# Kernel tuning notes

Measured on AMD Instinct MI355X. Metric: run time of the kernel, lower is better.

Reference implementation:

```python
import jax, jax.numpy as jnp
import numpy as np

B, L, H = 2, 2048, 2048
DI, N, DTR, K = 4096, 16, 128, 4  # intermediate, state, dt_rank, conv kernel


def setup_inputs() -> dict:
    key = jax.random.key(0)
    ks = jax.random.split(key, 8)
    x = jax.random.normal(ks[0], (B, L, H), jnp.float32)
    in_proj_w = jax.random.normal(ks[1], (2 * DI, H), jnp.float32) * 0.02
    conv1d_w = jax.random.normal(ks[2], (DI, 1, K), jnp.float32) * 0.1
    conv1d_b = jnp.zeros((DI,), jnp.float32)
    x_proj_w = jax.random.normal(ks[3], (DTR + 2 * N, DI), jnp.float32) * 0.02
    bound = DTR ** -0.5
    dt_proj_w = jax.random.uniform(ks[4], (DI, DTR), jnp.float32, -bound, bound)
    # faithful dt bias init: inverse-softplus of dt ~ Uniform-log[0.001, 0.1]
    dt = jnp.exp(jax.random.uniform(ks[5], (DI,), jnp.float32)
                 * (np.log(0.1) - np.log(0.001)) + np.log(0.001))
    dt = jnp.clip(dt, 1e-4)
    dt_proj_b = dt + jnp.log(-jnp.expm1(-dt))
    A_log = jnp.log(jnp.broadcast_to(jnp.arange(1, N + 1, dtype=jnp.float32), (DI, N)))
    D = jnp.ones((DI,), jnp.float32)
    out_proj_w = jax.random.normal(ks[6], (H, DI), jnp.float32) * 0.02
    return dict(x=x, in_proj_w=in_proj_w, conv1d_w=conv1d_w, conv1d_b=conv1d_b,
                x_proj_w=x_proj_w, dt_proj_w=dt_proj_w, dt_proj_b=dt_proj_b,
                A_log=A_log, D=D, out_proj_w=out_proj_w)


def _mamba_forward(x, in_proj_w, conv1d_w, conv1d_b, x_proj_w,
                   dt_proj_w, dt_proj_b, A_log, D, out_proj_w):
    # in_proj -> split into ssm input and gate (res)
    x_and_res = jnp.einsum('blh,eh->ble', x, in_proj_w)          # [B,L,2*DI]
    xi, res = jnp.split(x_and_res, 2, axis=-1)                    # [B,L,DI] each

    # depthwise causal conv1d (kernel K, left-pad K-1, truncated to L)
    xc = jnp.transpose(xi, (0, 2, 1))                             # [B,DI,L]
    xc = jax.lax.conv_general_dilated(
        xc, conv1d_w, window_strides=(1,), padding=((K - 1, 0),),
        dimension_numbers=('NCH', 'OIH', 'NCH'), feature_group_count=DI)
    xc = xc + conv1d_b[None, :, None]
    u = jax.nn.silu(jnp.transpose(xc, (0, 2, 1)))                 # [B,L,DI]

    # selective SSM parameters
    A = -jnp.exp(A_log.astype(jnp.float32))                       # [DI,N]
    x_dbl = jnp.einsum('bld,ed->ble', u, x_proj_w)                # [B,L,DTR+2N]
    dlt, Bm, Cm = jnp.split(x_dbl, [DTR, DTR + N], axis=-1)
    delta = jax.nn.softplus(jnp.einsum('blr,dr->bld', dlt, dt_proj_w) + dt_proj_b)

    # selective scan over time; carry h: [B,DI,N]
    def step(h, inp):
        d_t, B_t, C_t, u_t = inp                                  # [B,DI],[B,N],[B,N],[B,DI]
        dA = jnp.exp(d_t[:, :, None] * A)                         # [B,DI,N]
        h = dA * h + d_t[:, :, None] * B_t[:, None, :] * u_t[:, :, None]
        y_t = jnp.einsum('bdn,bn->bd', h, C_t)
        return h, y_t

    xs = (jnp.transpose(delta, (1, 0, 2)), jnp.transpose(Bm, (1, 0, 2)),
          jnp.transpose(Cm, (1, 0, 2)), jnp.transpose(u, (1, 0, 2)))
    h0 = jnp.zeros((x.shape[0], DI, N), jnp.float32)
    _, ys = jax.lax.scan(step, h0, xs)                            # ys: [L,B,DI]
    y = jnp.transpose(ys, (1, 0, 2)) + u * D.astype(jnp.float32)  # skip via D

    y = y * jax.nn.silu(res)                                      # gate
    return jnp.einsum('bld,hd->blh', y, out_proj_w)               # [B,L,H]


def reference(x, in_proj_w, conv1d_w, conv1d_b, x_proj_w,
              dt_proj_w, dt_proj_b, A_log, D, out_proj_w):
    return _mamba_forward(x, in_proj_w, conv1d_w, conv1d_b, x_proj_w,
                          dt_proj_w, dt_proj_b, A_log, D, out_proj_w)
```

## Files before the change

### kernel.cpp

```cpp
#include <hip/hip_runtime.h>
#include <hip/hip_bf16.h>
#include <stdint.h>

#define DEV static __device__ __forceinline__

typedef __attribute__((ext_vector_type(8))) short short8;
typedef __attribute__((ext_vector_type(4))) float f32x4;
typedef __attribute__((address_space(3))) void lds_void;
typedef __attribute__((address_space(1))) void glb_void;

constexpr int CB = 2, CL = 2048, CH = 2048, CDI = 4096, CN = 16, CDTR = 128;
constexpr int BLR = CB * CL;
constexpr int NC = 32, LC = 64;
constexpr int KSL = 8;

DEV ushort f2b(float f) {
  union { float f; uint32_t u; } v; v.f = f;
  uint32_t u = v.u;
  return (ushort)((u + 0x7fffu + ((u >> 16) & 1u)) >> 16);
}
DEV float b2f(ushort b) {
  union { uint32_t u; float f; } v; v.u = ((uint32_t)b) << 16;
  return v.f;
}
DEV void gload16(const ushort* g, ushort* l) {
  __builtin_amdgcn_global_load_lds((const glb_void*)g, (lds_void*)l, 16, 0, 0);
}

__global__ void cast_kernel(const float* __restrict__ in, ushort* __restrict__ out, int n4) {
  int i = blockIdx.x * blockDim.x + threadIdx.x;
  if (i >= n4) return;
  float4 v = *(const float4*)(in + (size_t)i * 4);
  *(ushort4*)(out + (size_t)i * 4) = make_ushort4(f2b(v.x), f2b(v.y), f2b(v.z), f2b(v.w));
}

__global__ void cast_pad_xproj_kernel(const float* __restrict__ in, ushort* __restrict__ out) {
  int i = blockIdx.x * blockDim.x + threadIdx.x;
  if (i >= (256 * 4096 / 4)) return;
  int idx = i * 4;
  int r = idx >> 12;
  ushort4 o;
  if (r < 160) {
    float4 v = *(const float4*)(in + idx);
    o = make_ushort4(f2b(v.x), f2b(v.y), f2b(v.z), f2b(v.w));
  } else {
    o = make_ushort4(0, 0, 0, 0);
  }
  *(ushort4*)(out + idx) = o;
}

__global__ void conv_silu_kernel(const ushort* __restrict__ xr, const float* __restrict__ w,
                                 const float* __restrict__ bias, ushort* __restrict__ u) {
  int t = blockIdx.x * blockDim.x + threadIdx.x;
  if (t >= BLR * CDI / 2) return;
  int d2 = t & (CDI / 2 - 1);
  int bl = t >> 11;
  int l = bl & (CL - 1);
  int d = d2 << 1;
  float4 w0 = *(const float4*)(w + (size_t)d * 4);
  float4 w1 = *(const float4*)(w + (size_t)d * 4 + 4);
  float wa0[4] = {w0.x, w0.y, w0.z, w0.w};
  float wa1[4] = {w1.x, w1.y, w1.z, w1.w};
  float a0 = bias[d], a1 = bias[d + 1];
#pragma unroll
  for (int k = 0; k < 4; ++k) {
    int ls = l - 3 + k;
    if (ls >= 0) {
      ushort2 xv = *(const ushort2*)(xr + (size_t)(bl - 3 + k) * 8192 + d);
      a0 = fmaf(wa0[k], b2f(xv.x), a0);
      a1 = fmaf(wa1[k], b2f(xv.y), a1);
    }
  }
  float s0 = a0 / (1.f + __expf(-a0));
  float s1 = a1 / (1.f + __expf(-a1));
  *(ushort2*)(u + (size_t)bl * 4096 + d) = make_ushort2(f2b(s0), f2b(s1));
}

template<int EPI>
__global__ __launch_bounds__(256, 4)
void gemm_bt_kernel(const ushort* __restrict__ A, const ushort* __restrict__ Bw,
                    void* __restrict__ Cp, const float* __restrict__ bias,
                    int M, int N, int K) {
  __shared__ ushort sA[128 * 32];
  __shared__ ushort sB[128 * 32];
  const int tid = threadIdx.x;
  const int bm = blockIdx.x, bn = blockIdx.y;
  const int w = tid >> 6, l = tid & 63;
  const int wr = w >> 1, wc = w & 1;
  const int q = l >> 4, r = l & 15;

  f32x4 acc[4][4] = {};

  const ushort* Ab = A + (size_t)bm * 128 * K;
  const ushort* Bb = Bw + (size_t)bn * 128 * K;
  const int nk = K >> 5;
  for (int kt = 0; kt < nk; ++kt) {
    const int k0 = kt << 5;
#pragma unroll
    for (int i = 0; i < 2; ++i) {
      const int chunk = i * 256 + tid;
      const int row = chunk >> 2;
      const int cofs = (chunk & 3) << 3;
      gload16(Ab + (size_t)row * K + k0 + cofs, sA + chunk * 8);
      gload16(Bb + (size_t)row * K + k0 + cofs, sB + chunk * 8);
    }
    __syncthreads();
    short8 af[4], bfg[4];
#pragma unroll
    for (int i = 0; i < 4; ++i) {
      af[i]  = *(const short8*)(sA + (wr * 64 + i * 16 + r) * 32 + q * 8);
      bfg[i] = *(const short8*)(sB + (wc * 64 + i * 16 + r) * 32 + q * 8);
    }
#pragma unroll
    for (int i = 0; i < 4; ++i)
#pragma unroll
      for (int j = 0; j < 4; ++j)
        acc[i][j] = __builtin_amdgcn_mfma_f32_16x16x32_bf16(af[i], bfg[j], acc[i][j], 0, 0, 0);
    __syncthreads();
  }

  const int m0 = bm * 128 + wr * 64;
  const int n0 = bn * 128 + wc * 64;
#pragma unroll
  for (int i = 0; i < 4; ++i) {
#pragma unroll
    for (int j = 0; j < 4; ++j) {
#pragma unroll
      for (int v = 0; v < 4; ++v) {
        const int grow = m0 + i * 16 + q * 4 + v;
        const int gcol = n0 + j * 16 + r;
        const float val = acc[i][j][v];
        if (EPI == 0) {
          ((ushort*)Cp)[(size_t)grow * N + gcol] = f2b(val);
        } else if (EPI == 1) {
          ((float*)Cp)[(size_t)grow * N + gcol] = val;
        } else {
          float xv = val + bias[gcol];
          float sp = xv > 20.f ? xv : log1pf(__expf(xv));
          ((ushort*)Cp)[(size_t)grow * N + gcol] = f2b(sp);
        }
      }
    }
  }
}

__global__ __launch_bounds__(256, 4)
void gemm_btk_kernel(const ushort* __restrict__ A, const ushort* __restrict__ Bw,
                     float* __restrict__ Cpart, int N, int Ktot, int Ksl) {
  __shared__ ushort sA[128 * 32];
  __shared__ ushort sB[128 * 32];
  const int tid = threadIdx.x;
  const int bm = blockIdx.x, bn = blockIdx.y, z = blockIdx.z;
  const int w = tid >> 6, l = tid & 63;
  const int wr = w >> 1, wc = w & 1;
  const int q = l >> 4, r = l & 15;

  f32x4 acc[4][4] = {};

  const ushort* Ab = A + (size_t)bm * 128 * Ktot + z * Ksl;
  const ushort* Bb = Bw + (size_t)bn * 128 * Ktot + z * Ksl;
  const int nk = Ksl >> 5;
  for (int kt = 0; kt < nk; ++kt) {
    const int k0 = kt << 5;
#pragma unroll
    for (int i = 0; i < 2; ++i) {
      const int chunk = i * 256 + tid;
      const int row = chunk >> 2;
      const int cofs = (chunk & 3) << 3;
      gload16(Ab + (size_t)row * Ktot + k0 + cofs, sA + chunk * 8);
      gload16(Bb + (size_t)row * Ktot + k0 + cofs, sB + chunk * 8);
    }
    __syncthreads();
    short8 af[4], bfg[4];
#pragma unroll
    for (int i = 0; i < 4; ++i) {
      af[i]  = *(const short8*)(sA + (wr * 64 + i * 16 + r) * 32 + q * 8);
      bfg[i] = *(const short8*)(sB + (wc * 64 + i * 16 + r) * 32 + q * 8);
    }
#pragma unroll
    for (int i = 0; i < 4; ++i)
#pragma unroll
      for (int j = 0; j < 4; ++j)
        acc[i][j] = __builtin_amdgcn_mfma_f32_16x16x32_bf16(af[i], bfg[j], acc[i][j], 0, 0, 0);
    __syncthreads();
  }

  float* Cz = Cpart + (size_t)z * BLR * N;
  const int m0 = bm * 128 + wr * 64;
  const int n0 = bn * 128 + wc * 64;
#pragma unroll
  for (int i = 0; i < 4; ++i)
#pragma unroll
    for (int j = 0; j < 4; ++j)
#pragma unroll
      for (int v = 0; v < 4; ++v)
        Cz[(size_t)(m0 + i * 16 + q * 4 + v) * N + (n0 + j * 16 + r)] = acc[i][j][v];
}

__global__ __launch_bounds__(256)
void reduce_xdbl_kernel(const float* __restrict__ part, float* __restrict__ xdbl,
                        ushort* __restrict__ dlt) {
  const int i = blockIdx.x * 256 + threadIdx.x;
  const int idx = i * 4;
  const int row = idx >> 8, col = idx & 255;
  float4 s = make_float4(0.f, 0.f, 0.f, 0.f);
#pragma unroll
  for (int z = 0; z < KSL; ++z) {
    float4 v = *(const float4*)(part + (size_t)z * BLR * 256 + idx);
    s.x += v.x; s.y += v.y; s.z += v.z; s.w += v.w;
  }
  *(float4*)(xdbl + idx) = s;
  if (col < 128) {
    *(ushort4*)(dlt + (size_t)row * 128 + col) =
        make_ushort4(f2b(s.x), f2b(s.y), f2b(s.z), f2b(s.w));
  }
}

__global__ __launch_bounds__(256)
void scan_pass1_kernel(const ushort* __restrict__ delta_bf, const ushort* __restrict__ u_bf,
                       const float* __restrict__ xdbl, const float* __restrict__ A_log,
                       float* __restrict__ Hc, float* __restrict__ Ssum) {
  __shared__ float4 sB[LC * 4];
  const int blk = blockIdx.x;
  const int dblk = blk & 15, bc = blk >> 4;
  const int b = bc & (CB - 1), c = bc >> 1;
  const int tid = threadIdx.x;
  const int d = dblk * 256 + tid;
  const size_t rowbase = (size_t)b * CL + c * LC;

  {
    const int rr = tid >> 2, seg = tid & 3;
    sB[tid] = *(const float4*)(xdbl + (rowbase + rr) * 256 + 128 + seg * 4);
  }
  __syncthreads();

  float Ae[16];
#pragma unroll
  for (int n = 0; n < 16; ++n) Ae[n] = -__expf(A_log[(size_t)d * CN + n]);
  float h[16] = {};
  float S = 0.f;
  for (int t = 0; t < LC; ++t) {
    const float dl = b2f(delta_bf[(rowbase + t) * 4096 + d]);
    const float uu = b2f(u_bf[(rowbase + t) * 4096 + d]);
    const float du = dl * uu;
    S += dl;
#pragma unroll
    for (int q = 0; q < 4; ++q) {
      float4 bq = sB[t * 4 + q];
      h[q * 4 + 0] = __expf(Ae[q * 4 + 0] * dl) * h[q * 4 + 0] + du * bq.x;
      h[q * 4 + 1] = __expf(Ae[q * 4 + 1] * dl) * h[q * 4 + 1] + du * bq.y;
      h[q * 4 + 2] = __expf(Ae[q * 4 + 2] * dl) * h[q * 4 + 2] + du * bq.z;
      h[q * 4 + 3] = __expf(Ae[q * 4 + 3] * dl) * h[q * 4 + 3] + du * bq.w;
    }
  }
  float4* Hp = (float4*)(Hc + ((((size_t)c * CB + b) * CDI + d) << 4));
#pragma unroll
  for (int q = 0; q < 4; ++q)
    Hp[q] = make_float4(h[q * 4 + 0], h[q * 4 + 1], h[q * 4 + 2], h[q * 4 + 3]);
  Ssum[((size_t)c * CB + b) * CDI + d] = S;
}

__global__ __launch_bounds__(256)
void scan_pass2_kernel(float* __restrict__ Hc, const float* __restrict__ Ssum,
                       const float* __restrict__ A_log) {
  const int t = blockIdx.x * 256 + threadIdx.x;
  const int n = t & 15, d = (t >> 4) & (CDI - 1), b = t >> 16;
  const float Ae = -__expf(A_log[(size_t)d * CN + n]);
  float h = 0.f;
  for (int c = 1; c < NC; ++c) {
    const size_t idxp = ((size_t)(c - 1) * CB + b) * CDI + d;
    const float P = __expf(Ae * Ssum[idxp]);
    h = P * h + Hc[idxp * 16 + n];
    Hc[idxp * 16 + n] = h;
  }
}

__global__ __launch_bounds__(256)
void scan_pass3_kernel(const ushort* __restrict__ delta_bf, const ushort* __restrict__ u_bf,
                       const float* __restrict__ xdbl, const ushort* __restrict__ xr,
                       const float* __restrict__ A_log, const float* __restrict__ Dvec,
                       const float* __restrict__ Hc, ushort* __restrict__ ybf) {
  __shared__ float4 sB[LC * 4];
  __shared__ float4 sC[LC * 4];
  const int blk = blockIdx.x;
  const int dblk = blk & 15, bc = blk >> 4;
  const int b = bc & (CB - 1), c = bc >> 1;
  const int tid = threadIdx.x;
  const int d = dblk * 256 + tid;
  const size_t rowbase = (size_t)b * CL + c * LC;

  {
    const int rr = tid >> 2, seg = tid & 3;
    sB[tid] = *(const float4*)(xdbl + (rowbase + rr) * 256 + 128 + seg * 4);
    sC[tid] = *(const float4*)(xdbl + (rowbase + rr) * 256 + 144 + seg * 4);
  }
  __syncthreads();

  float Ae[16];
#pragma unroll
  for (int n = 0; n < 16; ++n) Ae[n] = -__expf(A_log[(size_t)d * CN + n]);
  float h[16];
  if (c == 0) {
#pragma unroll
    for (int n = 0; n < 16; ++n) h[n] = 0.f;
  } else {
    const float4* Hp = (const float4*)(Hc + ((((size_t)(c - 1) * CB + b) * CDI + d) << 4));
#pragma unroll
    for (int q = 0; q < 4; ++q) {
      float4 hv = Hp[q];
      h[q * 4 + 0] = hv.x; h[q * 4 + 1] = hv.y; h[q * 4 + 2] = hv.z; h[q * 4 + 3] = hv.w;
    }
  }
  const float Dd = Dvec[d];
  for (int t = 0; t < LC; ++t) {
    const float dl = b2f(delta_bf[(rowbase + t) * 4096 + d]);
    const float uu = b2f(u_bf[(rowbase + t) * 4096 + d]);
    const float du = dl * uu;
    float y = 0.f;
#pragma unroll
    for (int q = 0; q < 4; ++q) {
      float4 bq = sB[t * 4 + q];
      float4 cq = sC[t * 4 + q];
      h[q * 4 + 0] = __expf(Ae[q * 4 + 0] * dl) * h[q * 4 + 0] + du * bq.x;
      h[q * 4 + 1] = __expf(Ae[q * 4 + 1] * dl) * h[q * 4 + 1] + du * bq.y;
      h[q * 4 + 2] = __expf(Ae[q * 4 + 2] * dl) * h[q * 4 + 2] + du * bq.z;
      h[q * 4 + 3] = __expf(Ae[q * 4 + 3] * dl) * h[q * 4 + 3] + du * bq.w;
      y = fmaf(h[q * 4 + 0], cq.x, y);
      y = fmaf(h[q * 4 + 1], cq.y, y);
      y = fmaf(h[q * 4 + 2], cq.z, y);
      y = fmaf(h[q * 4 + 3], cq.w, y);
    }
    const float res = b2f(xr[(rowbase + t) * 8192 + 4096 + d]);
    const float sres = res / (1.f + __expf(-res));
    ybf[(rowbase + t) * 4096 + d] = f2b((y + uu * Dd) * sres);
  }
}

extern "C" void kernel_launch(void* const* d_in, const int* in_sizes, int n_in,
                              void* d_out, int out_size, void* d_ws, size_t ws_size,
                              hipStream_t stream) {
  (void)in_sizes; (void)n_in; (void)out_size; (void)ws_size;
  const float* x       = (const float*)d_in[0];
  const float* in_w    = (const float*)d_in[1];
  const float* conv_w  = (const float*)d_in[2];
  const float* conv_b  = (const float*)d_in[3];
  const float* xproj_w = (const float*)d_in[4];
  const float* dt_w    = (const float*)d_in[5];
  const float* dt_b    = (const float*)d_in[6];
  const float* A_log   = (const float*)d_in[7];
  const float* Dvec    = (const float*)d_in[8];
  const float* out_w   = (const float*)d_in[9];
  float* out = (float*)d_out;
  char* ws = (char*)d_ws;
  const size_t MB = 1u << 20;

  ushort* xb    = (ushort*)(ws);
  float*  Hc    = (float*)(ws);
  ushort* wout  = (ushort*)(ws);
  ushort* wb1   = (ushort*)(ws + 16 * MB);
  ushort* u_bf  = (ushort*)(ws + 16 * MB);
  ushort* xr    = (ushort*)(ws + 48 * MB);
  float*  part  = (float*)(ws + 112 * MB);
  ushort* delta = (ushort*)(ws + 112 * MB);
  ushort* ybf   = (ushort*)(ws + 144 * MB);
  float*  xdbl  = (float*)(ws + 176 * MB);
  ushort* dlt   = (ushort*)(ws + 180 * MB);
  ushort* wxp   = (ushort*)(ws + 181 * MB);
  ushort* wdt   = (ushort*)(ws + 183 * MB);
  float*  Ssum  = (float*)(ws + 184 * MB);

  auto cast = [&](const float* in, ushort* o, int n) {
    cast_kernel<<<(n / 4 + 255) / 256, 256, 0, stream>>>(in, o, n / 4);
  };

  cast(x, xb, BLR * CH);
  cast(in_w, wb1, 2 * CDI * CH);
  gemm_bt_kernel<0><<<dim3(BLR / 128, (2 * CDI) / 128), 256, 0, stream>>>(
      xb, wb1, xr, nullptr, BLR, 2 * CDI, CH);
  conv_silu_kernel<<<(BLR * CDI / 2) / 256, 256, 0, stream>>>(xr, conv_w, conv_b, u_bf);
  cast_pad_xproj_kernel<<<(256 * 4096 / 4) / 256, 256, 0, stream>>>(xproj_w, wxp);
  gemm_btk_kernel<<<dim3(BLR / 128, 2, KSL), 256, 0, stream>>>(
      u_bf, wxp, part, 256, CDI, CDI / KSL);
  reduce_xdbl_kernel<<<(BLR * 256 / 4) / 256, 256, 0, stream>>>(part, xdbl, dlt);
  cast(dt_w, wdt, CDI * CDTR);
  gemm_bt_kernel<2><<<dim3(BLR / 128, CDI / 128), 256, 0, stream>>>(
      dlt, wdt, delta, dt_b, BLR, CDI, CDTR);
  scan_pass1_kernel<<<NC * CB * (CDI / 256), 256, 0, stream>>>(
      delta, u_bf, xdbl, A_log, Hc, Ssum);
  scan_pass2_kernel<<<(CB * CDI * CN) / 256, 256, 0, stream>>>(Hc, Ssum, A_log);
  scan_pass3_kernel<<<NC * CB * (CDI / 256), 256, 0, stream>>>(
      delta, u_bf, xdbl, xr, A_log, Dvec, Hc, ybf);
  cast(out_w, wout, CH * CDI);
  gemm_bt_kernel<1><<<dim3(BLR / 128, CH / 128), 256, 0, stream>>>(
      ybf, wout, out, nullptr, BLR, CH, CDI);
}
```

Before: 583.8 us.

## Use 256x256 double-buffered pipelined GEMM with swizzled LDS for in_proj

Adds a new 512-thread GEMM kernel with 256x256 output tiles, K-step 64, double-buffered LDS and XOR-swizzled layout. It interleaves the next tile's global-to-LDS loads with MFMA phases and uses raised wave priority. The kernel replaces the 128x128 single-buffer GEMM for the large in_proj matmul, aiming to hide load latency, raise data reuse and cut LDS bank conflicts. The cost is higher LDS and register use and an occupancy of one block per CU.

```diff
diff --git a/kernel.cpp b/kernel.cpp
--- a/kernel.cpp
+++ b/kernel.cpp
@@ -25,6 +25,9 @@
 }
 DEV void gload16(const ushort* g, ushort* l) {
   __builtin_amdgcn_global_load_lds((const glb_void*)g, (lds_void*)l, 16, 0, 0);
+}
+DEV f32x4 mfma16(short8 a, short8 b, f32x4 c) {
+  return __builtin_amdgcn_mfma_f32_16x16x32_bf16(a, b, c, 0, 0, 0);
 }
 
 __global__ void cast_kernel(const float* __restrict__ in, ushort* __restrict__ out, int n4) {
@@ -115,7 +118,7 @@
     for (int i = 0; i < 4; ++i)
 #pragma unroll
       for (int j = 0; j < 4; ++j)
-        acc[i][j] = __builtin_amdgcn_mfma_f32_16x16x32_bf16(af[i], bfg[j], acc[i][j], 0, 0, 0);
+        acc[i][j] = mfma16(af[i], bfg[j], acc[i][j]);
     __syncthreads();
   }
 
@@ -144,6 +147,108 @@
   }
 }
 
+template<int EPI>
+__global__ __launch_bounds__(512, 1)
+void gemm256p_kernel(const ushort* __restrict__ A, const ushort* __restrict__ Bw,
+                     void* __restrict__ Cp, int N, int K) {
+  __shared__ ushort sA[2][16384];
+  __shared__ ushort sB[2][16384];
+  const int tid = threadIdx.x;
+  const int bm = blockIdx.x, bn = blockIdx.y;
+  const int wid = tid >> 6, l = tid & 63;
+  const int wr = wid >> 2, wc = wid & 3;
+  const int q = l >> 4, r = l & 15;
+  const int rx = r & 7;
+  const int nt = K >> 6;
+
+  const ushort* Ab = A + (size_t)bm * 256 * K;
+  const ushort* Bb = Bw + (size_t)bn * 256 * K;
+
+  const int srow = tid >> 3;
+  const int sxor = (tid & 7) ^ (srow & 7);
+
+  auto stageA = [&](int T, int j) {
+    const int Ts = (T < nt) ? T : (nt - 1);
+    gload16(Ab + (size_t)(j * 64 + srow) * K + Ts * 64 + sxor * 8,
+            &sA[T & 1][0] + j * 4096 + tid * 8);
+  };
+  auto stageB = [&](int T, int j) {
+    const int Ts = (T < nt) ? T : (nt - 1);
+    gload16(Bb + (size_t)(j * 64 + srow) * K + Ts * 64 + sxor * 8,
+            &sB[T & 1][0] + j * 4096 + tid * 8);
+  };
+
+  const int sl0 = (q ^ rx) * 8;
+  const int sl1 = ((4 + q) ^ rx) * 8;
+
+  f32x4 acc[8][4] = {};
+
+  stageA(0, 1); stageA(0, 3);
+  stageB(0, 0); stageA(0, 0);
+  stageB(0, 2); stageA(0, 2);
+  stageB(0, 1); stageB(0, 3);
+  stageA(1, 1); stageA(1, 3);
+  asm volatile("s_waitcnt vmcnt(2)" ::: "memory");
+  __builtin_amdgcn_s_barrier();
+
+#define PHASE(M0, M1, S0, S1, LAST)                                        \
+  {                                                                        \
+    const int ra0 = (wr * 128 + (M0) * 16 + r) * 64;                       \
+    const int ra1 = (wr * 128 + (M1) * 16 + r) * 64;                       \
+    short8 a00 = *(const short8*)(At + ra0 + sl0);                         \
+    short8 a01 = *(const short8*)(At + ra0 + sl1);                         \
+    short8 a10 = *(const short8*)(At + ra1 + sl0);                         \
+    short8 a11 = *(const short8*)(At + ra1 + sl1);                         \
+    S0; S1;                                                                \
+    if (LAST) asm volatile("s_waitcnt vmcnt(2)" ::: "memory");             \
+    __builtin_amdgcn_s_barrier();                                          \
+    asm volatile("s_waitcnt lgkmcnt(0)" ::: "memory");                     \
+    __builtin_amdgcn_sched_barrier(0);                                     \
+    __builtin_amdgcn_s_setprio(1);                                         \
+    _Pragma("unroll")                                                      \
+    for (int n = 0; n < 4; ++n) {                                          \
+      acc[M0][n] = mfma16(a00, bf[n][0], acc[M0][n]);                      \
+      acc[M0][n] = mfma16(a01, bf[n][1], acc[M0][n]);                      \
+      acc[M1][n] = mfma16(a10, bf[n][0], acc[M1][n]);                      \
+      acc[M1][n] = mfma16(a11, bf[n][1], acc[M1][n]);                      \
+    }                                                                      \
+    __builtin_amdgcn_s_setprio(0);                                         \
+    __builtin_amdgcn_sched_barrier(0);                                     \
+    __builtin_amdgcn_s_barrier();                                          \
+  }
+
+  for (int t = 0; t < nt; ++t) {
+    const ushort* At = &sA[t & 1][0];
+    const ushort* Bt = &sB[t & 1][0];
+    short8 bf[4][2];
+#pragma unroll
+    for (int n = 0; n < 4; ++n) {
+      const int br = (wc * 64 + n * 16 + r) * 64;
+      bf[n][0] = *(const short8*)(Bt + br + sl0);
+      bf[n][1] = *(const short8*)(Bt + br + sl1);
+    }
+    PHASE(6, 7, stageB(t + 1, 0), stageA(t + 1, 0), false)
+    PHASE(4, 5, stageB(t + 1, 2), stageA(t + 1, 2), false)
+    PHASE(2, 3, stageB(t + 1, 1), stageB(t + 1, 3), false)
+    PHASE(0, 1, stageA(t + 2, 1), stageA(t + 2, 3), true)
+  }
+#undef PHASE
+
+  const int m0g = bm * 256 + wr * 128;
+  const int n0g = bn * 256 + wc * 64;
+#pragma unroll
+  for (int m = 0; m < 8; ++m)
+#pragma unroll
+    for (int n = 0; n < 4; ++n)
+#pragma unroll
+      for (int v = 0; v < 4; ++v) {
+        const int grow = m0g + m * 16 + q * 4 + v;
+        const int gcol = n0g + n * 16 + r;
+        if (EPI == 0) ((ushort*)Cp)[(size_t)grow * N + gcol] = f2b(acc[m][n][v]);
+        else          ((float*)Cp)[(size_t)grow * N + gcol]  = acc[m][n][v];
+      }
+}
+
 __global__ __launch_bounds__(256, 4)
 void gemm_btk_kernel(const ushort* __restrict__ A, const ushort* __restrict__ Bw,
                      float* __restrict__ Cpart, int N, int Ktot, int Ksl) {
@@ -181,7 +286,7 @@
     for (int i = 0; i < 4; ++i)
 #pragma unroll
       for (int j = 0; j < 4; ++j)
-        acc[i][j] = __builtin_amdgcn_mfma_f32_16x16x32_bf16(af[i], bfg[j], acc[i][j], 0, 0, 0);
+        acc[i][j] = mfma16(af[i], bfg[j], acc[i][j]);
     __syncthreads();
   }
 
@@ -375,8 +480,8 @@
 
   cast(x, xb, BLR * CH);
   cast(in_w, wb1, 2 * CDI * CH);
-  gemm_bt_kernel<0><<<dim3(BLR / 128, (2 * CDI) / 128), 256, 0, stream>>>(
-      xb, wb1, xr, nullptr, BLR, 2 * CDI, CH);
+  gemm256p_kernel<0><<<dim3(BLR / 256, (2 * CDI) / 256), 512, 0, stream>>>(
+      xb, wb1, xr, 2 * CDI, CH);
   conv_silu_kernel<<<(BLR * CDI / 2) / 256, 256, 0, stream>>>(xr, conv_w, conv_b, u_bf);
   cast_pad_xproj_kernel<<<(256 * 4096 / 4) / 256, 256, 0, stream>>>(xproj_w, wxp);
   gemm_btk_kernel<<<dim3(BLR / 128, 2, KSL), 256, 0, stream>>>(
```

After: 547.2 us. -6.3%, faster.
